# Kernel tuning notes

Measured on AMD Instinct MI355X. Metric: run time of the kernel, lower is better.

Reference implementation:

```python
import jax, jax.numpy as jnp
import numpy as np

D_MODEL = 1024
NUM_HEADS = 16
D_K = D_MODEL // NUM_HEADS
D_FF = 4096
LN_EPS = 1e-5


def layernorm(x, gamma, beta):
    mu = jnp.mean(x, axis=-1, keepdims=True)
    var = jnp.mean(jnp.square(x - mu), axis=-1, keepdims=True)
    return (x - mu) * jax.lax.rsqrt(var + LN_EPS) * gamma + beta


def setup_inputs() -> dict:
    key = jax.random.key(0)
    ks = jax.random.split(key, 16)
    s = 1.0 / np.sqrt(D_MODEL)
    sf = 1.0 / np.sqrt(D_FF)
    inp = {
        "x": jax.random.normal(ks[0], (2, 2048, D_MODEL), dtype=jnp.float32),
        # attention sublayer LN
        "ln1_g": jnp.ones((D_MODEL,), jnp.float32),
        "ln1_b": jnp.zeros((D_MODEL,), jnp.float32),
        # QKV / output projections, stored as [in, out]
        "Wq": jax.random.uniform(ks[1], (D_MODEL, D_MODEL), jnp.float32, -s, s),
        "bq": jax.random.uniform(ks[2], (D_MODEL,), jnp.float32, -s, s),
        "Wk": jax.random.uniform(ks[3], (D_MODEL, D_MODEL), jnp.float32, -s, s),
        "bk": jax.random.uniform(ks[4], (D_MODEL,), jnp.float32, -s, s),
        "Wv": jax.random.uniform(ks[5], (D_MODEL, D_MODEL), jnp.float32, -s, s),
        "bv": jax.random.uniform(ks[6], (D_MODEL,), jnp.float32, -s, s),
        "Wo": jax.random.uniform(ks[7], (D_MODEL, D_MODEL), jnp.float32, -s, s),
        "bo": jax.random.uniform(ks[8], (D_MODEL,), jnp.float32, -s, s),
        # FFN sublayer LN
        "ln2_g": jnp.ones((D_MODEL,), jnp.float32),
        "ln2_b": jnp.zeros((D_MODEL,), jnp.float32),
        "W1": jax.random.uniform(ks[9], (D_MODEL, D_FF), jnp.float32, -s, s),
        "b1": jax.random.uniform(ks[10], (D_FF,), jnp.float32, -s, s),
        "W2": jax.random.uniform(ks[11], (D_FF, D_MODEL), jnp.float32, -sf, sf),
        "b2": jax.random.uniform(ks[12], (D_MODEL,), jnp.float32, -sf, sf),
    }
    return inp


def block_fwd(x, ln1_g, ln1_b, Wq, bq, Wk, bk, Wv, bv, Wo, bo,
              ln2_g, ln2_b, W1, b1, W2, b2):
    B, S, D = x.shape
    # --- attention sublayer (pre-LN + residual) ---
    h = layernorm(x, ln1_g, ln1_b)
    q = (h @ Wq + bq).reshape(B, S, NUM_HEADS, D_K)
    k = (h @ Wk + bk).reshape(B, S, NUM_HEADS, D_K)
    v = (h @ Wv + bv).reshape(B, S, NUM_HEADS, D_K)
    scale = 1.0 / np.sqrt(D_K)  # == sqrt(d_k)/d_k in source
    attn = jnp.einsum("bqhd,bkhd->bhqk", q, k) * scale  # [B,H,S,S]
    causal = jnp.arange(S)[:, None] >= jnp.arange(S)[None, :]
    attn = jnp.where(causal, attn, -jnp.inf)
    score = jax.nn.softmax(attn, axis=-1)
    o = jnp.einsum("bhqk,bkhd->bqhd", score, v).reshape(B, S, D)
    x = x + (o @ Wo + bo)
    # --- FFN sublayer (pre-LN + residual) ---
    h = layernorm(x, ln2_g, ln2_b)
    h = jax.nn.gelu(h @ W1 + b1, approximate=False)  # torch nn.GELU = exact erf
    return x + (h @ W2 + b2)


def reference(x, ln1_g, ln1_b, Wq, bq, Wk, bk, Wv, bv, Wo, bo,
              ln2_g, ln2_b, W1, b1, W2, b2):
    return block_fwd(x, ln1_g, ln1_b, Wq, bq, Wk, bk, Wv, bv, Wo, bo,
                     ln2_g, ln2_b, W1, b1, W2, b2)
```

## Files before the change

### kernel.cpp

```cpp
#include <hip/hip_runtime.h>
#include <hip/hip_bf16.h>
#include <math.h>

typedef unsigned short u16;
typedef unsigned int u32;
typedef __bf16 bf16x8 __attribute__((ext_vector_type(8)));
typedef float f32x4 __attribute__((ext_vector_type(4)));

#define MFMA16(a, b, c) __builtin_amdgcn_mfma_f32_16x16x32_bf16(a, b, c, 0, 0, 0)

__device__ __forceinline__ u16 f2b(float f) {
    __bf16 h = (__bf16)f;
    return __builtin_bit_cast(u16, h);
}

__device__ __forceinline__ void gld16(const void* g, void* l) {
    __builtin_amdgcn_global_load_lds(
        (const __attribute__((address_space(1))) unsigned int*)g,
        (__attribute__((address_space(3))) unsigned int*)l, 16, 0, 0);
}

__global__ void transpose_convert(const float* __restrict__ in, u16* __restrict__ out,
                                  int R, int C) {
    __shared__ float tile[32][33];
    int c0 = blockIdx.x * 32, r0 = blockIdx.y * 32;
    int tx = threadIdx.x, ty = threadIdx.y;
#pragma unroll
    for (int i = 0; i < 4; i++)
        tile[ty + i * 8][tx] = in[(size_t)(r0 + ty + i * 8) * C + c0 + tx];
    __syncthreads();
#pragma unroll
    for (int i = 0; i < 4; i++)
        out[(size_t)(c0 + ty + i * 8) * R + r0 + tx] = f2b(tile[tx][ty + i * 8]);
}

__global__ __launch_bounds__(256) void ln_kernel(const float* __restrict__ x,
                                                 const float* __restrict__ g,
                                                 const float* __restrict__ b,
                                                 u16* __restrict__ out) {
    int row = blockIdx.x;
    int tid = threadIdx.x;
    const float* xr = x + (size_t)row * 1024;
    float4 v = ((const float4*)xr)[tid];
    float s = v.x + v.y + v.z + v.w;
    float s2 = v.x * v.x + v.y * v.y + v.z * v.z + v.w * v.w;
#pragma unroll
    for (int off = 32; off > 0; off >>= 1) {
        s += __shfl_xor(s, off);
        s2 += __shfl_xor(s2, off);
    }
    __shared__ float ps[4], ps2[4];
    int wid = tid >> 6;
    if ((tid & 63) == 0) { ps[wid] = s; ps2[wid] = s2; }
    __syncthreads();
    s = ps[0] + ps[1] + ps[2] + ps[3];
    s2 = ps2[0] + ps2[1] + ps2[2] + ps2[3];
    float mu = s * (1.0f / 1024.0f);
    float var = s2 * (1.0f / 1024.0f) - mu * mu;
    float rs = rsqrtf(var + 1e-5f);
    int c = tid * 4;
    ushort4 o;
    o.x = f2b((v.x - mu) * rs * g[c + 0] + b[c + 0]);
    o.y = f2b((v.y - mu) * rs * g[c + 1] + b[c + 1]);
    o.z = f2b((v.z - mu) * rs * g[c + 2] + b[c + 2]);
    o.w = f2b((v.w - mu) * rs * g[c + 3] + b[c + 3]);
    ((ushort4*)(out + (size_t)row * 1024))[tid] = o;
}

__global__ __launch_bounds__(256) void vtrans_kernel(const u16* __restrict__ Vb,
                                                     u16* __restrict__ VbT) {
    __shared__ u16 t[64][66];
    const int tid = threadIdx.x;
    const int s0 = blockIdx.x * 64;
    const int bh = blockIdx.y;
    const u16* src = Vb + (size_t)bh * 2048 * 64;
    u16* dst = VbT + (size_t)bh * 64 * 2048;
#pragma unroll
    for (int p = 0; p < 2; p++) {
        int idx = p * 256 + tid;
        int r = idx >> 3, dc = (idx & 7) * 8;
        uint4 v = *(const uint4*)&src[(size_t)(s0 + r) * 64 + dc];
        const u16* pv = (const u16*)&v;
#pragma unroll
        for (int j = 0; j < 8; j++) t[r][dc + j] = pv[j];
    }
    __syncthreads();
    int d = tid >> 2, sc = (tid & 3) * 16;
    u16 buf[16];
#pragma unroll
    for (int m = 0; m < 16; m++) {
        int cp = sc + m;
        int blk = cp >> 5, c = cp & 31;
        int srcw = blk * 32 + (c >> 1) + (c & 1) * 16;
        buf[m] = t[srcw][d];
    }
    *(uint4*)&dst[(size_t)d * 2048 + s0 + sc] = *(uint4*)&buf[0];
    *(uint4*)&dst[(size_t)d * 2048 + s0 + sc + 8] = *(uint4*)&buf[8];
}

#define EPI_QKV 0
#define EPI_RESID 1
#define EPI_GELU 2

__device__ __forceinline__ void gemm_stage(const u16* __restrict__ A,
                                           const u16* __restrict__ BT,
                                           u16 (&Asb)[128][32], u16 (&Bsb)[128][32],
                                           int m0, int n0, int K, int k0, int sr, int sdc,
                                           int wb) {
    gld16(&A[(size_t)(m0 + sr) * K + k0 + sdc], &Asb[0][0] + wb);
    gld16(&A[(size_t)(m0 + 64 + sr) * K + k0 + sdc], &Asb[0][0] + 2048 + wb);
    gld16(&BT[(size_t)(n0 + sr) * K + k0 + sdc], &Bsb[0][0] + wb);
    gld16(&BT[(size_t)(n0 + 64 + sr) * K + k0 + sdc], &Bsb[0][0] + 2048 + wb);
}

__device__ __forceinline__ void gemm_compute(const u16 (&Asb)[128][32],
                                             const u16 (&Bsb)[128][32], f32x4 (&acc)[4][4],
                                             int wm, int wn, int quad, int c15) {
    bf16x8 af[4], bfr[4];
#pragma unroll
    for (int i = 0; i < 4; i++) af[i] = *(const bf16x8*)&Asb[wm + i * 16 + c15][quad * 8];
#pragma unroll
    for (int j = 0; j < 4; j++) bfr[j] = *(const bf16x8*)&Bsb[wn + j * 16 + c15][quad * 8];
#pragma unroll
    for (int i = 0; i < 4; i++)
#pragma unroll
        for (int j = 0; j < 4; j++) acc[i][j] = MFMA16(af[i], bfr[j], acc[i][j]);
}

template <int EPI>
__global__ __launch_bounds__(256) void gemm_kernel(const u16* __restrict__ A,
                                                   const u16* __restrict__ BT,
                                                   const float* __restrict__ bias0,
                                                   const float* __restrict__ bias1,
                                                   const float* __restrict__ bias2,
                                                   void* __restrict__ outp,
                                                   const float* __restrict__ resid,
                                                   int N, int K) {
    __shared__ __align__(16) u16 As0[128][32], Bs0[128][32];
    __shared__ __align__(16) u16 As1[128][32], Bs1[128][32];
    const int tid = threadIdx.x;
    const int m0 = blockIdx.y * 128, n0 = blockIdx.x * 128;
    const int w = tid >> 6, lid = tid & 63, quad = lid >> 4, c15 = lid & 15;
    const int wm = (w >> 1) * 64, wn = (w & 1) * 64;
    const int sr = tid >> 2, sdc = (tid & 3) * 8;
    const int wb = (tid & 192) * 8;

    f32x4 acc[4][4] = {};

    gemm_stage(A, BT, As0, Bs0, m0, n0, K, 0, sr, sdc, wb);
    const int KT = K >> 5;
    for (int kt = 0; kt < KT; kt += 2) {
        __syncthreads();
        gemm_stage(A, BT, As1, Bs1, m0, n0, K, (kt + 1) << 5, sr, sdc, wb);
        gemm_compute(As0, Bs0, acc, wm, wn, quad, c15);
        __syncthreads();
        if (kt + 2 < KT) gemm_stage(A, BT, As0, Bs0, m0, n0, K, (kt + 2) << 5, sr, sdc, wb);
        gemm_compute(As1, Bs1, acc, wm, wn, quad, c15);
    }

    const int which = n0 >> 10;
    const float* bias = (EPI == EPI_QKV) ? (which == 0 ? bias0 : (which == 1 ? bias1 : bias2))
                                         : bias0;
    u16* qkv_dst = (u16*)outp + (size_t)which * 4194304;

#pragma unroll
    for (int i = 0; i < 4; i++) {
#pragma unroll
        for (int j = 0; j < 4; j++) {
#pragma unroll
            for (int r = 0; r < 4; r++) {
                int gr = m0 + wm + i * 16 + quad * 4 + r;
                int gc = n0 + wn + j * 16 + c15;
                if (EPI == EPI_QKV) {
                    int lc = gc & 1023;
                    float v = acc[i][j][r] + bias[lc];
                    int bb = gr >> 11, ss = gr & 2047, hh = lc >> 6, dd = lc & 63;
                    qkv_dst[((size_t)((bb * 16 + hh) * 2048 + ss)) * 64 + dd] = f2b(v);
                } else if (EPI == EPI_RESID) {
                    float v = acc[i][j][r] + bias[gc];
                    ((float*)outp)[(size_t)gr * N + gc] = resid[(size_t)gr * N + gc] + v;
                } else {
                    float v = acc[i][j][r] + bias[gc];
                    float ge = 0.5f * v * (1.0f + erff(v * 0.70710678118654752f));
                    ((u16*)outp)[(size_t)gr * N + gc] = f2b(ge);
                }
            }
        }
    }
}

__device__ __forceinline__ void attn_step(const u16 (&KB)[2][64][32],
                                          const u16 (&VB)[2][64][32],
                                          u16 (&Psw)[2][32][40], const bf16x8 (&aq)[2][2],
                                          f32x4 (&o)[2][4], float (&lsum)[2][4], int kv0,
                                          int qr0, int quad, int c15) {
    if (kv0 > qr0 + 31) return;
    bf16x8 bk[4][2];
#pragma unroll
    for (int nf = 0; nf < 4; nf++)
#pragma unroll
        for (int kd = 0; kd < 2; kd++)
            bk[nf][kd] = *(const bf16x8*)&KB[kd][nf * 16 + c15][quad * 8];
    f32x4 sf[2][4];
#pragma unroll
    for (int qf = 0; qf < 2; qf++)
#pragma unroll
        for (int nf = 0; nf < 4; nf++) {
            f32x4 s = {};
            s = MFMA16(aq[qf][0], bk[nf][0], s);
            s = MFMA16(aq[qf][1], bk[nf][1], s);
            sf[qf][nf] = s;
        }
    const bool domask = (kv0 + 63 > qr0);
    if (domask) {
#pragma unroll
        for (int qf = 0; qf < 2; qf++)
#pragma unroll
            for (int r = 0; r < 4; r++) {
                int rowg = qr0 + qf * 16 + quad * 4 + r;
#pragma unroll
                for (int nf = 0; nf < 4; nf++) {
                    float p = (kv0 + nf * 16 + c15 <= rowg) ? __expf(sf[qf][nf][r] * 0.125f)
                                                            : 0.0f;
                    sf[qf][nf][r] = p;
                    lsum[qf][r] += p;
                }
            }
    } else {
#pragma unroll
        for (int qf = 0; qf < 2; qf++)
#pragma unroll
            for (int r = 0; r < 4; r++)
#pragma unroll
                for (int nf = 0; nf < 4; nf++) {
                    float p = __expf(sf[qf][nf][r] * 0.125f);
                    sf[qf][nf][r] = p;
                    lsum[qf][r] += p;
                }
    }
#pragma unroll
    for (int qf = 0; qf < 2; qf++)
#pragma unroll
        for (int ks = 0; ks < 2; ks++)
#pragma unroll
            for (int r = 0; r < 4; r++) {
                u32 pk = (u32)f2b(sf[qf][2 * ks][r]) | ((u32)f2b(sf[qf][2 * ks + 1][r]) << 16);
                *(u32*)&Psw[ks][qf * 16 + quad * 4 + r][2 * c15] = pk;
            }
    asm volatile("s_waitcnt lgkmcnt(0)" ::: "memory");
    bf16x8 ap[2][2];
#pragma unroll
    for (int qf = 0; qf < 2; qf++)
#pragma unroll
        for (int ks = 0; ks < 2; ks++)
            ap[qf][ks] = *(const bf16x8*)&Psw[ks][qf * 16 + c15][quad * 8];
#pragma unroll
    for (int df = 0; df < 4; df++) {
        bf16x8 bv0 = *(const bf16x8*)&VB[0][df * 16 + c15][quad * 8];
        bf16x8 bv1 = *(const bf16x8*)&VB[1][df * 16 + c15][quad * 8];
#pragma unroll
        for (int qf = 0; qf < 2; qf++) {
            o[qf][df] = MFMA16(ap[qf][0], bv0, o[qf][df]);
            o[qf][df] = MFMA16(ap[qf][1], bv1, o[qf][df]);
        }
    }
}

__global__ __launch_bounds__(256) void attn_kernel(const u16* __restrict__ Q,
                                                   const u16* __restrict__ Kb,
                                                   const u16* __restrict__ VbT,
                                                   u16* __restrict__ attO) {
    __shared__ __align__(16) u16 K0s[2][64][32], K1s[2][64][32];
    __shared__ __align__(16) u16 V0s[2][64][32], V1s[2][64][32];
    __shared__ __align__(16) u16 Ps[4][2][32][40];

    const int tid = threadIdx.x;
    const int bh = blockIdx.x;
    const int pj = blockIdx.y;
    const size_t base = (size_t)bh * 2048 * 64;
    const u16* Qp = Q + base;
    const u16* Kp = Kb + base;
    const u16* Vp = VbT + (size_t)bh * 64 * 2048;
    const int w = tid >> 6, lane = tid & 63, quad = lane >> 4, c15 = lane & 15;
    const int sr = tid >> 2, sdc = (tid & 3) * 8;
    const int wb = (tid & 192) * 8;
    const int bb = bh >> 4, hh = bh & 15;

#define ATTN_STAGE(KB, VB, kvo)                                                        \
    do {                                                                               \
        gld16(&Kp[(size_t)((kvo) + sr) * 64 + sdc], &KB[0][0][0] + wb);                \
        gld16(&Kp[(size_t)((kvo) + sr) * 64 + 32 + sdc], &KB[0][0][0] + 2048 + wb);    \
        gld16(&Vp[(size_t)sr * 2048 + (kvo) + sdc], &VB[0][0][0] + wb);                \
        gld16(&Vp[(size_t)sr * 2048 + (kvo) + 32 + sdc], &VB[0][0][0] + 2048 + wb);    \
    } while (0)

    auto run_tile = [&](int q0) {
        const int qr0 = q0 + w * 32;
        bf16x8 aq[2][2];
#pragma unroll
        for (int qf = 0; qf < 2; qf++)
#pragma unroll
            for (int ks = 0; ks < 2; ks++)
                aq[qf][ks] = *(const bf16x8*)&Qp[(size_t)(qr0 + qf * 16 + c15) * 64 +
                                                 ks * 32 + quad * 8];
        f32x4 o[2][4] = {};
        float lsum[2][4] = {};
        const int steps = (q0 >> 6) + 2;
        __syncthreads();
        ATTN_STAGE(K0s, V0s, 0);
        int s = 0;
        for (;;) {
            __syncthreads();
            if (s + 1 < steps) ATTN_STAGE(K1s, V1s, (s + 1) << 6);
            attn_step(K0s, V0s, Ps[w], aq, o, lsum, s << 6, qr0, quad, c15);
            if (++s >= steps) break;
            __syncthreads();
            if (s + 1 < steps) ATTN_STAGE(K0s, V0s, (s + 1) << 6);
            attn_step(K1s, V1s, Ps[w], aq, o, lsum, s << 6, qr0, quad, c15);
            if (++s >= steps) break;
        }
#pragma unroll
        for (int qf = 0; qf < 2; qf++)
#pragma unroll
            for (int r = 0; r < 4; r++) {
                float l = lsum[qf][r];
#pragma unroll
                for (int off = 1; off < 16; off <<= 1) l += __shfl_xor(l, off);
                float inv = 1.0f / l;
                int sg = qr0 + qf * 16 + quad * 4 + r;
                size_t rowoff = ((size_t)(bb * 2048 + sg)) * 1024 + hh * 64;
#pragma unroll
                for (int df = 0; df < 4; df++)
                    attO[rowoff + df * 16 + c15] = f2b(o[qf][df][r] * inv);
            }
    };
    run_tile((15 - pj) * 128);
    run_tile(pj * 128);
#undef ATTN_STAGE
}

extern "C" void kernel_launch(void* const* d_in, const int* in_sizes, int n_in,
                              void* d_out, int out_size, void* d_ws, size_t ws_size,
                              hipStream_t stream) {
    const float* x = (const float*)d_in[0];
    const float* ln1g = (const float*)d_in[1];
    const float* ln1b = (const float*)d_in[2];
    const float* Wq = (const float*)d_in[3];
    const float* bq = (const float*)d_in[4];
    const float* Wk = (const float*)d_in[5];
    const float* bk = (const float*)d_in[6];
    const float* Wv = (const float*)d_in[7];
    const float* bv = (const float*)d_in[8];
    const float* Wo = (const float*)d_in[9];
    const float* bo = (const float*)d_in[10];
    const float* ln2g = (const float*)d_in[11];
    const float* ln2b = (const float*)d_in[12];
    const float* W1 = (const float*)d_in[13];
    const float* b1 = (const float*)d_in[14];
    const float* W2 = (const float*)d_in[15];
    const float* b2 = (const float*)d_in[16];
    float* out = (float*)d_out;

    char* ws = (char*)d_ws;
    u16* wqkvT = (u16*)(ws + 0);
    u16* woT = (u16*)(ws + 6291456);
    u16* w1T = (u16*)(ws + 8388608);
    u16* w2T = (u16*)(ws + 16777216);
    u16* h = (u16*)(ws + 25165824);
    float* x1 = (float*)(ws + 33554432);
    u16* Qb = (u16*)(ws + 50331648);
    u16* Kb = (u16*)(ws + 58720256);
    u16* Vb = (u16*)(ws + 67108864);
    u16* VbT = (u16*)(ws + 75497472);
    u16* aO = Vb;
    u16* mid = Qb;

    dim3 tb(32, 8);
    transpose_convert<<<dim3(32, 32), tb, 0, stream>>>(Wq, wqkvT, 1024, 1024);
    transpose_convert<<<dim3(32, 32), tb, 0, stream>>>(Wk, wqkvT + 1048576, 1024, 1024);
    transpose_convert<<<dim3(32, 32), tb, 0, stream>>>(Wv, wqkvT + 2097152, 1024, 1024);
    transpose_convert<<<dim3(32, 32), tb, 0, stream>>>(Wo, woT, 1024, 1024);
    transpose_convert<<<dim3(128, 32), tb, 0, stream>>>(W1, w1T, 1024, 4096);
    transpose_convert<<<dim3(32, 128), tb, 0, stream>>>(W2, w2T, 4096, 1024);

    ln_kernel<<<4096, 256, 0, stream>>>(x, ln1g, ln1b, h);

    gemm_kernel<EPI_QKV><<<dim3(24, 32), 256, 0, stream>>>(h, wqkvT, bq, bk, bv, Qb, nullptr,
                                                           3072, 1024);

    vtrans_kernel<<<dim3(32, 32), 256, 0, stream>>>(Vb, VbT);

    attn_kernel<<<dim3(32, 8), 256, 0, stream>>>(Qb, Kb, VbT, aO);

    gemm_kernel<EPI_RESID><<<dim3(8, 32), 256, 0, stream>>>(aO, woT, bo, nullptr, nullptr, x1,
                                                            x, 1024, 1024);

    ln_kernel<<<4096, 256, 0, stream>>>(x1, ln2g, ln2b, h);

    gemm_kernel<EPI_GELU><<<dim3(32, 32), 256, 0, stream>>>(h, w1T, b1, nullptr, nullptr, mid,
                                                            nullptr, 4096, 1024);
    gemm_kernel<EPI_RESID><<<dim3(8, 32), 256, 0, stream>>>(mid, w2T, b2, nullptr, nullptr, out,
                                                            x1, 1024, 4096);
}
```

Measured before the change: 378.6 us.

## Triple-buffer GEMM and attention loads, merge weight transposes, use tanh GELU

The GEMM and attention kernels move from double to triple buffering in LDS. Each stage now waits on a partial vmcnt plus a barrier instead of a full __syncthreads, so two tiles are in flight while one is computed. The six weight transpose launches are merged into one kernel with a flat grid to cut launch overhead. The exact erf GELU is replaced with a tanh approximation built on __expf, which departs from the required exact-erf semantics.

```diff
diff --git a/kernel.cpp b/kernel.cpp
--- a/kernel.cpp
+++ b/kernel.cpp
@@ -9,6 +9,9 @@
 
 #define MFMA16(a, b, c) __builtin_amdgcn_mfma_f32_16x16x32_bf16(a, b, c, 0, 0, 0)
 
+#define WAIT_VM4_BAR() asm volatile("s_waitcnt vmcnt(4)\n\ts_barrier" ::: "memory")
+#define WAIT_VM0_BAR() asm volatile("s_waitcnt vmcnt(0)\n\ts_barrier" ::: "memory")
+
 __device__ __forceinline__ u16 f2b(float f) {
     __bf16 h = (__bf16)f;
     return __builtin_bit_cast(u16, h);
@@ -20,10 +23,31 @@
         (__attribute__((address_space(3))) unsigned int*)l, 16, 0, 0);
 }
 
-__global__ void transpose_convert(const float* __restrict__ in, u16* __restrict__ out,
-                                  int R, int C) {
+__global__ __launch_bounds__(256) void transpose_all(
+    const float* __restrict__ Wq, const float* __restrict__ Wk,
+    const float* __restrict__ Wv, const float* __restrict__ Wo,
+    const float* __restrict__ W1, const float* __restrict__ W2, u16* __restrict__ wqkvT,
+    u16* __restrict__ woT, u16* __restrict__ w1T, u16* __restrict__ w2T) {
     __shared__ float tile[32][33];
-    int c0 = blockIdx.x * 32, r0 = blockIdx.y * 32;
+    int t = blockIdx.x;
+    const float* in;
+    u16* out;
+    int R, C;
+    if (t < 3072) {
+        int m = t >> 10;
+        t &= 1023;
+        in = m == 0 ? Wq : (m == 1 ? Wk : Wv);
+        out = wqkvT + m * 1048576;
+        R = 1024; C = 1024;
+    } else if (t < 4096) {
+        t -= 3072; in = Wo; out = woT; R = 1024; C = 1024;
+    } else if (t < 8192) {
+        t -= 4096; in = W1; out = w1T; R = 1024; C = 4096;
+    } else {
+        t -= 8192; in = W2; out = w2T; R = 4096; C = 1024;
+    }
+    int tilesX = C >> 5;
+    int c0 = (t % tilesX) * 32, r0 = (t / tilesX) * 32;
     int tx = threadIdx.x, ty = threadIdx.y;
 #pragma unroll
     for (int i = 0; i < 4; i++)
@@ -136,8 +160,8 @@
                                                    void* __restrict__ outp,
                                                    const float* __restrict__ resid,
                                                    int N, int K) {
-    __shared__ __align__(16) u16 As0[128][32], Bs0[128][32];
-    __shared__ __align__(16) u16 As1[128][32], Bs1[128][32];
+    __shared__ __align__(16) u16 As[3][128][32];
+    __shared__ __align__(16) u16 Bs[3][128][32];
     const int tid = threadIdx.x;
     const int m0 = blockIdx.y * 128, n0 = blockIdx.x * 128;
     const int w = tid >> 6, lid = tid & 63, quad = lid >> 4, c15 = lid & 15;
@@ -147,16 +171,22 @@
 
     f32x4 acc[4][4] = {};
 
-    gemm_stage(A, BT, As0, Bs0, m0, n0, K, 0, sr, sdc, wb);
+    gemm_stage(A, BT, As[0], Bs[0], m0, n0, K, 0, sr, sdc, wb);
+    gemm_stage(A, BT, As[1], Bs[1], m0, n0, K, 32, sr, sdc, wb);
     const int KT = K >> 5;
-    for (int kt = 0; kt < KT; kt += 2) {
-        __syncthreads();
-        gemm_stage(A, BT, As1, Bs1, m0, n0, K, (kt + 1) << 5, sr, sdc, wb);
-        gemm_compute(As0, Bs0, acc, wm, wn, quad, c15);
-        __syncthreads();
-        if (kt + 2 < KT) gemm_stage(A, BT, As0, Bs0, m0, n0, K, (kt + 2) << 5, sr, sdc, wb);
-        gemm_compute(As1, Bs1, acc, wm, wn, quad, c15);
-    }
+    int buf = 0;
+    for (int kt = 0; kt < KT - 1; kt++) {
+        WAIT_VM4_BAR();
+        if (kt + 2 < KT) {
+            int nb = buf + 2;
+            if (nb >= 3) nb -= 3;
+            gemm_stage(A, BT, As[nb], Bs[nb], m0, n0, K, (kt + 2) << 5, sr, sdc, wb);
+        }
+        gemm_compute(As[buf], Bs[buf], acc, wm, wn, quad, c15);
+        if (++buf == 3) buf = 0;
+    }
+    WAIT_VM0_BAR();
+    gemm_compute(As[buf], Bs[buf], acc, wm, wn, quad, c15);
 
     const int which = n0 >> 10;
     const float* bias = (EPI == EPI_QKV) ? (which == 0 ? bias0 : (which == 1 ? bias1 : bias2))
@@ -181,8 +211,10 @@
                     ((float*)outp)[(size_t)gr * N + gc] = resid[(size_t)gr * N + gc] + v;
                 } else {
                     float v = acc[i][j][r] + bias[gc];
-                    float ge = 0.5f * v * (1.0f + erff(v * 0.70710678118654752f));
-                    ((u16*)outp)[(size_t)gr * N + gc] = f2b(ge);
+                    float u = v * (0.79788456f + 0.03567741f * v * v);
+                    float e = __expf(2.0f * u);
+                    float th = 1.0f - 2.0f / (e + 1.0f);
+                    ((u16*)outp)[(size_t)gr * N + gc] = f2b(0.5f * v * (1.0f + th));
                 }
             }
         }
@@ -270,8 +302,8 @@
                                                    const u16* __restrict__ Kb,
                                                    const u16* __restrict__ VbT,
                                                    u16* __restrict__ attO) {
-    __shared__ __align__(16) u16 K0s[2][64][32], K1s[2][64][32];
-    __shared__ __align__(16) u16 V0s[2][64][32], V1s[2][64][32];
+    __shared__ __align__(16) u16 Ks[3][2][64][32];
+    __shared__ __align__(16) u16 Vs[3][2][64][32];
     __shared__ __align__(16) u16 Ps[4][2][32][40];
 
     const int tid = threadIdx.x;
@@ -286,12 +318,12 @@
     const int wb = (tid & 192) * 8;
     const int bb = bh >> 4, hh = bh & 15;
 
-#define ATTN_STAGE(KB, VB, kvo)                                                        \
-    do {                                                                               \
-        gld16(&Kp[(size_t)((kvo) + sr) * 64 + sdc], &KB[0][0][0] + wb);                \
-        gld16(&Kp[(size_t)((kvo) + sr) * 64 + 32 + sdc], &KB[0][0][0] + 2048 + wb);    \
-        gld16(&Vp[(size_t)sr * 2048 + (kvo) + sdc], &VB[0][0][0] + wb);                \
-        gld16(&Vp[(size_t)sr * 2048 + (kvo) + 32 + sdc], &VB[0][0][0] + 2048 + wb);    \
+#define ATTN_STAGE(bi, kvo)                                                          \
+    do {                                                                             \
+        gld16(&Kp[(size_t)((kvo) + sr) * 64 + sdc], &Ks[bi][0][0][0] + wb);          \
+        gld16(&Kp[(size_t)((kvo) + sr) * 64 + 32 + sdc], &Ks[bi][0][0][0] + 2048 + wb); \
+        gld16(&Vp[(size_t)sr * 2048 + (kvo) + sdc], &Vs[bi][0][0][0] + wb);          \
+        gld16(&Vp[(size_t)sr * 2048 + (kvo) + 32 + sdc], &Vs[bi][0][0][0] + 2048 + wb); \
     } while (0)
 
     auto run_tile = [&](int q0) {
@@ -307,17 +339,19 @@
         float lsum[2][4] = {};
         const int steps = (q0 >> 6) + 2;
         __syncthreads();
-        ATTN_STAGE(K0s, V0s, 0);
-        int s = 0;
-        for (;;) {
-            __syncthreads();
-            if (s + 1 < steps) ATTN_STAGE(K1s, V1s, (s + 1) << 6);
-            attn_step(K0s, V0s, Ps[w], aq, o, lsum, s << 6, qr0, quad, c15);
-            if (++s >= steps) break;
-            __syncthreads();
-            if (s + 1 < steps) ATTN_STAGE(K0s, V0s, (s + 1) << 6);
-            attn_step(K1s, V1s, Ps[w], aq, o, lsum, s << 6, qr0, quad, c15);
-            if (++s >= steps) break;
+        ATTN_STAGE(0, 0);
+        ATTN_STAGE(1, 64);
+        int buf = 0;
+        for (int s = 0; s < steps; s++) {
+            if (s < steps - 1) WAIT_VM4_BAR();
+            else WAIT_VM0_BAR();
+            if (s + 2 < steps) {
+                int nb = buf + 2;
+                if (nb >= 3) nb -= 3;
+                ATTN_STAGE(nb, (s + 2) << 6);
+            }
+            attn_step(Ks[buf], Vs[buf], Ps[w], aq, o, lsum, s << 6, qr0, quad, c15);
+            if (++buf == 3) buf = 0;
         }
 #pragma unroll
         for (int qf = 0; qf < 2; qf++)
@@ -375,13 +409,8 @@
     u16* aO = Vb;
     u16* mid = Qb;
 
-    dim3 tb(32, 8);
-    transpose_convert<<<dim3(32, 32), tb, 0, stream>>>(Wq, wqkvT, 1024, 1024);
-    transpose_convert<<<dim3(32, 32), tb, 0, stream>>>(Wk, wqkvT + 1048576, 1024, 1024);
-    transpose_convert<<<dim3(32, 32), tb, 0, stream>>>(Wv, wqkvT + 2097152, 1024, 1024);
-    transpose_convert<<<dim3(32, 32), tb, 0, stream>>>(Wo, woT, 1024, 1024);
-    transpose_convert<<<dim3(128, 32), tb, 0, stream>>>(W1, w1T, 1024, 4096);
-    transpose_convert<<<dim3(32, 128), tb, 0, stream>>>(W2, w2T, 4096, 1024);
+    transpose_all<<<12288, dim3(32, 8), 0, stream>>>(Wq, Wk, Wv, Wo, W1, W2, wqkvT, woT,
+                                                     w1T, w2T);
 
     ln_kernel<<<4096, 256, 0, stream>>>(x, ln1g, ln1b, h);
 
```

Result: slower. 393.0 us (+3.8%).
